# Optimization experiments

Measured on AMD Instinct MI355X. Metric: run time of the kernel, lower is better.

The kernel has to match this reference:

```python
import math
import jax, jax.numpy as jnp
import numpy as np

NUM_BINS = 8
TRANS = 8
LEFT, RIGHT = -1.0, 1.0
MIN_W = MIN_H = MIN_D = 1.0e-4


def setup_inputs() -> dict:
    key = jax.random.key(0)
    ks = jax.random.split(key, 8)
    B, D, H, OUT = 524288, 16, 256, TRANS * (3 * NUM_BINS - 1)
    x = jax.random.uniform(ks[0], (B, D), jnp.float32, -0.99, 0.99)
    W0 = jax.random.normal(ks[1], (8, H), jnp.float32) * (1.0 / math.sqrt(8))
    b0 = jnp.zeros((H,), jnp.float32)
    W1 = jax.random.normal(ks[2], (H, H), jnp.float32) * (1.0 / math.sqrt(H))
    b1 = jnp.zeros((H,), jnp.float32)
    Wout = jax.random.normal(ks[3], (H, OUT), jnp.float32) * (0.1 / math.sqrt(H))
    bout = jnp.zeros((OUT,), jnp.float32)
    return {"x": x, "W0": W0, "b0": b0, "W1": W1, "b1": b1, "Wout": Wout, "bout": bout}


def _rq_spline(x, raw_w, raw_h, raw_d):
    # x: [B, T]; raw_w/raw_h: [B, T, K]; raw_d: [B, T, K-1]
    span = RIGHT - LEFT
    const = math.log(math.exp(1.0 - MIN_D) - 1.0)
    widths = jax.nn.softmax(raw_w, axis=-1)
    heights = jax.nn.softmax(raw_h, axis=-1)
    derivs = jax.nn.softplus(raw_d + const) + MIN_D
    widths = span * (MIN_W + (1.0 - MIN_W * NUM_BINS) * widths)
    heights = span * (MIN_H + (1.0 - MIN_H * NUM_BINS) * heights)
    edge_x = LEFT + jnp.pad(jnp.cumsum(widths, axis=-1), ((0, 0), (0, 0), (1, 0)))
    edge_y = LEFT + jnp.pad(jnp.cumsum(heights, axis=-1), ((0, 0), (0, 0), (1, 0)))
    derivs = jnp.pad(derivs, ((0, 0), (0, 0), (1, 1)), constant_values=1.0)
    out_mask = (x <= LEFT + 1e-3) | (x >= RIGHT - 1e-3)
    x_in = jnp.where(out_mask, 0.0, x)
    # searchsorted(right=True) - 1 == count of edges <= x_in, minus 1
    idx = jnp.clip(jnp.sum(edge_x <= x_in[..., None], axis=-1) - 1, 0, NUM_BINS - 1)
    g = lambda a: jnp.take_along_axis(a, idx[..., None], axis=-1)[..., 0]
    xk, yk = g(edge_x), g(edge_y)
    wk, hk = g(widths), g(heights)
    dk, dk1 = g(derivs), g(derivs[..., 1:])
    sk = hk / wk
    eps = (x_in - xk) / wk
    eps_term = eps * (1.0 - eps)
    eps2 = eps * eps
    beta = sk + (dk1 + dk - 2.0 * sk) * eps_term
    alpha = hk * (sk * eps2 + dk * eps_term)
    output = jnp.where(out_mask, x, yk + alpha / beta)
    logdet = (2.0 * jnp.log(sk)
              + jnp.log(dk1 * eps2 + 2.0 * sk * eps_term + dk * (1.0 - eps) ** 2)
              - 2.0 * jnp.log(beta))
    logdet = jnp.where(out_mask, 0.0, logdet)
    return output, logdet


def reference(x, W0, b0, W1, b1, Wout, bout):
    x1 = x[..., :TRANS]   # transformed half (mask == True)
    x2 = x[..., TRANS:]   # conditioning half
    h = jax.nn.relu(x2 @ W0 + b0)
    h = jax.nn.relu(h @ W1 + b1)
    raw = (h @ Wout + bout).reshape(x.shape[0], TRANS, 3 * NUM_BINS - 1)
    raw_w = raw[..., :NUM_BINS]
    raw_h = raw[..., NUM_BINS:2 * NUM_BINS]
    raw_d = raw[..., 2 * NUM_BINS:]
    y1, logdet = _rq_spline(x1, raw_w, raw_h, raw_d)
    out = jnp.concatenate([y1, x2], axis=-1)
    return out, jnp.sum(logdet, axis=-1)
```

## Files before the change

kernel.cpp:

```cpp
#include <hip/hip_runtime.h>
#include <hip/hip_bf16.h>


typedef __bf16 bf16x8 __attribute__((ext_vector_type(8)));
typedef __bf16 bf16x4 __attribute__((ext_vector_type(4)));
typedef float  f32x4  __attribute__((ext_vector_type(4)));

#define MFMA16(a,b,c) __builtin_amdgcn_mfma_f32_16x16x32_bf16((a),(b),(c),0,0,0)

#define SW_W1_OFF 8192
#define SW_WO_OFF 73728
#define SW_TOTAL  122880

#define HSTRIDE 264

__global__ void prep_kernel(const float* __restrict__ W0,
                            const float* __restrict__ W1,
                            const float* __restrict__ Wout,
                            __bf16* __restrict__ sw)
{
  int i = blockIdx.x * 256 + threadIdx.x;
  if (i >= SW_TOTAL) return;
  const float* src; int K, N, NT, li;
  if (i < SW_W1_OFF)      { src = W0;   K = 8;   N = 256; NT = 16; li = i; }
  else if (i < SW_WO_OFF) { src = W1;   K = 256; N = 256; NT = 16; li = i - SW_W1_OFF; }
  else                    { src = Wout; K = 256; N = 184; NT = 12; li = i - SW_WO_OFF; }
  int j    = li & 7;
  int l    = (li >> 3) & 63;
  int rest = li >> 9;
  int nt   = rest % NT;
  int kb   = rest / NT;
  int k = kb * 32 + ((l >> 4) << 3) + j;
  int n = nt * 16 + (l & 15);
  float v = (k < K && n < N) ? src[k * N + n] : 0.0f;
  sw[i] = (__bf16)v;
}

__global__ __launch_bounds__(512, 4)
void fused_kernel(const float* __restrict__ x,
                  const float* __restrict__ b0v,
                  const float* __restrict__ b1v,
                  const float* __restrict__ boutv,
                  const __bf16* __restrict__ sw,
                  float* __restrict__ out,
                  int nrows)
{
  __shared__ __align__(16) unsigned char smem[2 * 64 * HSTRIDE * 2];
  __bf16* h1   = (__bf16*)smem;
  __bf16* h2   = (__bf16*)(smem + 64 * HSTRIDE * 2);
  __bf16* rawb = h1;
  float*  ldet = (float*)h2;

  const int tid  = threadIdx.x;
  const int wave = tid >> 6;
  const int lane = tid & 63;
  const int quad = lane >> 4;
  const int l16  = lane & 15;
  const int row0 = blockIdx.x * 64;

  const __bf16* swW1 = sw + SW_W1_OFF;
  const __bf16* swWo = sw + SW_WO_OFF;
  const f32x4 z4 = {0.f, 0.f, 0.f, 0.f};

  const int mq = wave >> 1;
  const int nh = wave & 1;

  {
    bf16x8 bfr[2];
    #pragma unroll
    for (int nt = 0; nt < 2; nt++){
      bf16x8 b = {};
      if (quad == 0){
        const float* xp = x + (long)(row0 + (nh*2 + nt)*16 + l16)*16 + 8;
        float4 u = *(const float4*)xp;
        float4 v = *(const float4*)(xp + 4);
        b[0]=(__bf16)u.x; b[1]=(__bf16)u.y; b[2]=(__bf16)u.z; b[3]=(__bf16)u.w;
        b[4]=(__bf16)v.x; b[5]=(__bf16)v.y; b[6]=(__bf16)v.z; b[7]=(__bf16)v.w;
      }
      bfr[nt] = b;
    }
    #pragma unroll
    for (int mi = 0; mi < 4; mi++){
      int mt = mq*4 + mi;
      bf16x8 a = *(const bf16x8*)(sw + (mt*64 + lane)*8);
      f32x4 acc0 = MFMA16(a, bfr[0], z4);
      f32x4 acc1 = MFMA16(a, bfr[1], z4);
      float4 bb = *(const float4*)(b0v + mt*16 + quad*4);
      bf16x4 p0, p1;
      p0[0]=(__bf16)fmaxf(acc0[0]+bb.x,0.f); p0[1]=(__bf16)fmaxf(acc0[1]+bb.y,0.f);
      p0[2]=(__bf16)fmaxf(acc0[2]+bb.z,0.f); p0[3]=(__bf16)fmaxf(acc0[3]+bb.w,0.f);
      p1[0]=(__bf16)fmaxf(acc1[0]+bb.x,0.f); p1[1]=(__bf16)fmaxf(acc1[1]+bb.y,0.f);
      p1[2]=(__bf16)fmaxf(acc1[2]+bb.z,0.f); p1[3]=(__bf16)fmaxf(acc1[3]+bb.w,0.f);
      *(bf16x4*)(h1 + ((nh*2+0)*16 + l16)*HSTRIDE + mt*16 + quad*4) = p0;
      *(bf16x4*)(h1 + ((nh*2+1)*16 + l16)*HSTRIDE + mt*16 + quad*4) = p1;
    }
  }
  __syncthreads();

  {
    f32x4 acc[4][2];
    #pragma unroll
    for (int mi=0;mi<4;mi++){ acc[mi][0]=z4; acc[mi][1]=z4; }
    #pragma unroll
    for (int kb=0;kb<8;kb++){
      bf16x8 bfr[2];
      #pragma unroll
      for (int nt=0;nt<2;nt++)
        bfr[nt] = *(const bf16x8*)(h1 + ((nh*2+nt)*16 + l16)*HSTRIDE + kb*32 + quad*8);
      #pragma unroll
      for (int mi=0;mi<4;mi++){
        bf16x8 a = *(const bf16x8*)(swW1 + ((kb*16 + mq*4 + mi)*64 + lane)*8);
        acc[mi][0] = MFMA16(a, bfr[0], acc[mi][0]);
        acc[mi][1] = MFMA16(a, bfr[1], acc[mi][1]);
      }
    }
    #pragma unroll
    for (int mi=0;mi<4;mi++){
      int mt = mq*4 + mi;
      float4 bb = *(const float4*)(b1v + mt*16 + quad*4);
      #pragma unroll
      for (int nt=0;nt<2;nt++){
        bf16x4 p;
        p[0]=(__bf16)fmaxf(acc[mi][nt][0]+bb.x,0.f);
        p[1]=(__bf16)fmaxf(acc[mi][nt][1]+bb.y,0.f);
        p[2]=(__bf16)fmaxf(acc[mi][nt][2]+bb.z,0.f);
        p[3]=(__bf16)fmaxf(acc[mi][nt][3]+bb.w,0.f);
        *(bf16x4*)(h2 + ((nh*2+nt)*16 + l16)*HSTRIDE + mt*16 + quad*4) = p;
      }
    }
  }
  __syncthreads();

  {
    const int mh = wave >> 2;
    const int nc = wave & 3;
    f32x4 acc[2][3];
    #pragma unroll
    for (int mi=0;mi<2;mi++)
      #pragma unroll
      for (int ni=0;ni<3;ni++) acc[mi][ni] = z4;
    #pragma unroll
    for (int kb=0;kb<8;kb++){
      bf16x8 af[2];
      #pragma unroll
      for (int mi=0;mi<2;mi++)
        af[mi] = *(const bf16x8*)(h2 + ((mh*2+mi)*16 + l16)*HSTRIDE + kb*32 + quad*8);
      #pragma unroll
      for (int ni=0;ni<3;ni++){
        bf16x8 b = *(const bf16x8*)(swWo + ((kb*12 + nc*3 + ni)*64 + lane)*8);
        acc[0][ni] = MFMA16(af[0], b, acc[0][ni]);
        acc[1][ni] = MFMA16(af[1], b, acc[1][ni]);
      }
    }
    #pragma unroll
    for (int ni=0;ni<3;ni++){
      int col = (nc*3 + ni)*16 + l16;
      if (col < 184){
        int t = (col * 713) >> 14;
        float bias = boutv[col];
        #pragma unroll
        for (int mi=0;mi<2;mi++)
          #pragma unroll
          for (int r=0;r<4;r++){
            int row = (mh*2+mi)*16 + quad*4 + r;
            rawb[row*HSTRIDE + col + t] = (__bf16)(acc[mi][ni][r] + bias);
          }
      }
    }
  }
  __syncthreads();

  {
    int row = tid >> 3;
    int t   = tid & 7;
    long gr = row0 + row;
    float xv = x[gr*16 + t];
    out[gr*16 + 8 + t] = x[gr*16 + 8 + t];

    const __bf16* rr = rawb + row*HSTRIDE + t*24;
    bf16x8 v0 = *(const bf16x8*)(rr);
    bf16x8 v1 = *(const bf16x8*)(rr + 8);
    bf16x8 v2 = *(const bf16x8*)(rr + 16);

    float ew[8], eh[8];
    float sw_ = 0.f, sh_ = 0.f;
    #pragma unroll
    for (int i=0;i<8;i++){ ew[i] = __expf((float)v0[i]); sw_ += ew[i]; }
    #pragma unroll
    for (int i=0;i<8;i++){ eh[i] = __expf((float)v1[i]); sh_ += eh[i]; }
    float cw = 1.9984f * __builtin_amdgcn_rcpf(sw_);
    float ch = 1.9984f * __builtin_amdgcn_rcpf(sh_);

    float d[9];
    d[0] = 1.f; d[8] = 1.f;
    #pragma unroll
    for (int i=0;i<7;i++){
      float z = (float)v2[i] + 0.54116666f;
      d[i+1] = fmaxf(z, 0.f) + __logf(1.f + __expf(-fabsf(z))) + 1e-4f;
    }

    bool msk = (xv <= -0.999f) || (xv >= 0.999f);
    float xin = msk ? 0.f : xv;

    float w_i = fmaf(ew[0], cw, 2e-4f);
    float h_i = fmaf(eh[0], ch, 2e-4f);
    float edge = -1.f + w_i, cy = -1.f + h_i;
    float xk = -1.f, yk = -1.f, wk = w_i, hk = h_i, dk = d[0], dk1 = d[1];
    #pragma unroll
    for (int i=1;i<8;i++){
      w_i = fmaf(ew[i], cw, 2e-4f);
      h_i = fmaf(eh[i], ch, 2e-4f);
      bool le = (edge <= xin);
      xk  = le ? edge : xk;
      yk  = le ? cy   : yk;
      wk  = le ? w_i  : wk;
      hk  = le ? h_i  : hk;
      dk  = le ? d[i] : dk;
      dk1 = le ? d[i+1] : dk1;
      edge += w_i; cy += h_i;
    }

    float rwk = __builtin_amdgcn_rcpf(wk);
    float sk  = hk * rwk;
    float eps = (xin - xk) * rwk;
    float om  = 1.f - eps;
    float et  = eps * om;
    float e2  = eps * eps;
    float beta  = sk + (dk1 + dk - 2.f*sk) * et;
    float rb    = __builtin_amdgcn_rcpf(beta);
    float alpha = hk * (sk*e2 + dk*et);
    float yv  = msk ? xv : (yk + alpha * rb);
    float num = dk1*e2 + 2.f*sk*et + dk*om*om;
    float arg = sk*sk*num*rb*rb;
    float ld  = msk ? 0.f : __logf(arg);

    out[gr*16 + t] = yv;
    ldet[tid] = ld;
  }
  __syncthreads();

  if (tid < 64){
    float s = 0.f;
    #pragma unroll
    for (int t=0;t<8;t++) s += ldet[tid*8 + t];
    out[(long)nrows*16 + row0 + tid] = s;
  }
}

extern "C" void kernel_launch(void* const* d_in, const int* in_sizes, int n_in,
                              void* d_out, int out_size, void* d_ws, size_t ws_size,
                              hipStream_t stream)
{
  const float* x    = (const float*)d_in[0];
  const float* W0   = (const float*)d_in[1];
  const float* b0   = (const float*)d_in[2];
  const float* W1   = (const float*)d_in[3];
  const float* b1   = (const float*)d_in[4];
  const float* Wout = (const float*)d_in[5];
  const float* bout = (const float*)d_in[6];
  float* out = (float*)d_out;
  __bf16* sw = (__bf16*)d_ws;

  int nrows = in_sizes[0] / 16;
  int ntiles = nrows / 64;

  prep_kernel<<<(SW_TOTAL + 255)/256, 256, 0, stream>>>(W0, W1, Wout, sw);
  fused_kernel<<<ntiles, 512, 0, stream>>>(x, b0, b1, bout, sw, out, nrows);
}
```

Baseline: 265.6 us.

## Halve rows per block to 32 and raise occupancy target to 8 blocks

Each block now processes 32 rows instead of 64. The wave-to-tile mapping is reworked so every wave covers all rows of layers 0 and 1 for two output tiles, and the output-layer tiles are split unevenly across waves (2,2,2,2,1,1,1,1). Shared memory is halved and launch bounds ask for 8 blocks per CU, aiming at more resident waves to hide latency. The spline epilogue now uses only 256 threads while the other 256 copy the passthrough half. In exchange, each weight fragment loaded from global/L2 feeds half as many MFMAs, the output layer is load-imbalanced across waves, and register pressure must fit the tighter bound.

New measurement: 276.1 us. 3.9% more time.

```diff
diff --git a/kernel.cpp b/kernel.cpp
--- a/kernel.cpp
+++ b/kernel.cpp
@@ -12,6 +12,7 @@
 #define SW_WO_OFF 73728
 #define SW_TOTAL  122880
 
+#define ROWS    32
 #define HSTRIDE 264
 
 __global__ void prep_kernel(const float* __restrict__ W0,
@@ -36,7 +37,7 @@
   sw[i] = (__bf16)v;
 }
 
-__global__ __launch_bounds__(512, 4)
+__global__ __launch_bounds__(512, 8)
 void fused_kernel(const float* __restrict__ x,
                   const float* __restrict__ b0v,
                   const float* __restrict__ b1v,
@@ -45,9 +46,9 @@
                   float* __restrict__ out,
                   int nrows)
 {
-  __shared__ __align__(16) unsigned char smem[2 * 64 * HSTRIDE * 2];
+  __shared__ __align__(16) unsigned char smem[2 * ROWS * HSTRIDE * 2];
   __bf16* h1   = (__bf16*)smem;
-  __bf16* h2   = (__bf16*)(smem + 64 * HSTRIDE * 2);
+  __bf16* h2   = (__bf16*)(smem + ROWS * HSTRIDE * 2);
   __bf16* rawb = h1;
   float*  ldet = (float*)h2;
 
@@ -56,22 +57,19 @@
   const int lane = tid & 63;
   const int quad = lane >> 4;
   const int l16  = lane & 15;
-  const int row0 = blockIdx.x * 64;
+  const int row0 = blockIdx.x * ROWS;
 
   const __bf16* swW1 = sw + SW_W1_OFF;
   const __bf16* swWo = sw + SW_WO_OFF;
   const f32x4 z4 = {0.f, 0.f, 0.f, 0.f};
 
-  const int mq = wave >> 1;
-  const int nh = wave & 1;
-
   {
     bf16x8 bfr[2];
     #pragma unroll
     for (int nt = 0; nt < 2; nt++){
       bf16x8 b = {};
       if (quad == 0){
-        const float* xp = x + (long)(row0 + (nh*2 + nt)*16 + l16)*16 + 8;
+        const float* xp = x + (long)(row0 + nt*16 + l16)*16 + 8;
         float4 u = *(const float4*)xp;
         float4 v = *(const float4*)(xp + 4);
         b[0]=(__bf16)u.x; b[1]=(__bf16)u.y; b[2]=(__bf16)u.z; b[3]=(__bf16)u.w;
@@ -80,8 +78,8 @@
       bfr[nt] = b;
     }
     #pragma unroll
-    for (int mi = 0; mi < 4; mi++){
-      int mt = mq*4 + mi;
+    for (int mi = 0; mi < 2; mi++){
+      int mt = wave*2 + mi;
       bf16x8 a = *(const bf16x8*)(sw + (mt*64 + lane)*8);
       f32x4 acc0 = MFMA16(a, bfr[0], z4);
       f32x4 acc1 = MFMA16(a, bfr[1], z4);
@@ -91,32 +89,32 @@
       p0[2]=(__bf16)fmaxf(acc0[2]+bb.z,0.f); p0[3]=(__bf16)fmaxf(acc0[3]+bb.w,0.f);
       p1[0]=(__bf16)fmaxf(acc1[0]+bb.x,0.f); p1[1]=(__bf16)fmaxf(acc1[1]+bb.y,0.f);
       p1[2]=(__bf16)fmaxf(acc1[2]+bb.z,0.f); p1[3]=(__bf16)fmaxf(acc1[3]+bb.w,0.f);
-      *(bf16x4*)(h1 + ((nh*2+0)*16 + l16)*HSTRIDE + mt*16 + quad*4) = p0;
-      *(bf16x4*)(h1 + ((nh*2+1)*16 + l16)*HSTRIDE + mt*16 + quad*4) = p1;
+      *(bf16x4*)(h1 + (0*16 + l16)*HSTRIDE + mt*16 + quad*4) = p0;
+      *(bf16x4*)(h1 + (1*16 + l16)*HSTRIDE + mt*16 + quad*4) = p1;
     }
   }
   __syncthreads();
 
   {
-    f32x4 acc[4][2];
-    #pragma unroll
-    for (int mi=0;mi<4;mi++){ acc[mi][0]=z4; acc[mi][1]=z4; }
+    f32x4 acc[2][2];
+    #pragma unroll
+    for (int mi=0;mi<2;mi++){ acc[mi][0]=z4; acc[mi][1]=z4; }
     #pragma unroll
     for (int kb=0;kb<8;kb++){
       bf16x8 bfr[2];
       #pragma unroll
       for (int nt=0;nt<2;nt++)
-        bfr[nt] = *(const bf16x8*)(h1 + ((nh*2+nt)*16 + l16)*HSTRIDE + kb*32 + quad*8);
-      #pragma unroll
-      for (int mi=0;mi<4;mi++){
-        bf16x8 a = *(const bf16x8*)(swW1 + ((kb*16 + mq*4 + mi)*64 + lane)*8);
+        bfr[nt] = *(const bf16x8*)(h1 + (nt*16 + l16)*HSTRIDE + kb*32 + quad*8);
+      #pragma unroll
+      for (int mi=0;mi<2;mi++){
+        bf16x8 a = *(const bf16x8*)(swW1 + ((kb*16 + wave*2 + mi)*64 + lane)*8);
         acc[mi][0] = MFMA16(a, bfr[0], acc[mi][0]);
         acc[mi][1] = MFMA16(a, bfr[1], acc[mi][1]);
       }
     }
     #pragma unroll
-    for (int mi=0;mi<4;mi++){
-      int mt = mq*4 + mi;
+    for (int mi=0;mi<2;mi++){
+      int mt = wave*2 + mi;
       float4 bb = *(const float4*)(b1v + mt*16 + quad*4);
       #pragma unroll
       for (int nt=0;nt<2;nt++){
@@ -125,44 +123,44 @@
         p[1]=(__bf16)fmaxf(acc[mi][nt][1]+bb.y,0.f);
         p[2]=(__bf16)fmaxf(acc[mi][nt][2]+bb.z,0.f);
         p[3]=(__bf16)fmaxf(acc[mi][nt][3]+bb.w,0.f);
-        *(bf16x4*)(h2 + ((nh*2+nt)*16 + l16)*HSTRIDE + mt*16 + quad*4) = p;
+        *(bf16x4*)(h2 + (nt*16 + l16)*HSTRIDE + mt*16 + quad*4) = p;
       }
     }
   }
   __syncthreads();
 
   {
-    const int mh = wave >> 2;
-    const int nc = wave & 3;
-    f32x4 acc[2][3];
-    #pragma unroll
-    for (int mi=0;mi<2;mi++)
-      #pragma unroll
-      for (int ni=0;ni<3;ni++) acc[mi][ni] = z4;
+    const int ncnt = (wave < 4) ? 2 : 1;
+    const int nbase = (wave < 4) ? wave*2 : wave + 4;
+    f32x4 acc[2][2];
+    #pragma unroll
+    for (int mi=0;mi<2;mi++){ acc[mi][0]=z4; acc[mi][1]=z4; }
     #pragma unroll
     for (int kb=0;kb<8;kb++){
       bf16x8 af[2];
       #pragma unroll
       for (int mi=0;mi<2;mi++)
-        af[mi] = *(const bf16x8*)(h2 + ((mh*2+mi)*16 + l16)*HSTRIDE + kb*32 + quad*8);
-      #pragma unroll
-      for (int ni=0;ni<3;ni++){
-        bf16x8 b = *(const bf16x8*)(swWo + ((kb*12 + nc*3 + ni)*64 + lane)*8);
-        acc[0][ni] = MFMA16(af[0], b, acc[0][ni]);
-        acc[1][ni] = MFMA16(af[1], b, acc[1][ni]);
-      }
-    }
-    #pragma unroll
-    for (int ni=0;ni<3;ni++){
-      int col = (nc*3 + ni)*16 + l16;
-      if (col < 184){
+        af[mi] = *(const bf16x8*)(h2 + (mi*16 + l16)*HSTRIDE + kb*32 + quad*8);
+      #pragma unroll
+      for (int ni=0;ni<2;ni++){
+        if (ni < ncnt){
+          bf16x8 b = *(const bf16x8*)(swWo + ((kb*12 + nbase + ni)*64 + lane)*8);
+          acc[0][ni] = MFMA16(af[0], b, acc[0][ni]);
+          acc[1][ni] = MFMA16(af[1], b, acc[1][ni]);
+        }
+      }
+    }
+    #pragma unroll
+    for (int ni=0;ni<2;ni++){
+      int col = (nbase + ni)*16 + l16;
+      if (ni < ncnt && col < 184){
         int t = (col * 713) >> 14;
         float bias = boutv[col];
         #pragma unroll
         for (int mi=0;mi<2;mi++)
           #pragma unroll
           for (int r=0;r<4;r++){
-            int row = (mh*2+mi)*16 + quad*4 + r;
+            int row = mi*16 + quad*4 + r;
             rawb[row*HSTRIDE + col + t] = (__bf16)(acc[mi][ni][r] + bias);
           }
       }
@@ -170,12 +168,11 @@
   }
   __syncthreads();
 
-  {
+  if (tid < 256){
     int row = tid >> 3;
     int t   = tid & 7;
     long gr = row0 + row;
     float xv = x[gr*16 + t];
-    out[gr*16 + 8 + t] = x[gr*16 + 8 + t];
 
     const __bf16* rr = rawb + row*HSTRIDE + t*24;
     bf16x8 v0 = *(const bf16x8*)(rr);
@@ -236,10 +233,15 @@
 
     out[gr*16 + t] = yv;
     ldet[tid] = ld;
-  }
-  __syncthreads();
-
-  if (tid < 64){
+  } else {
+    int p   = tid - 256;
+    long gr = row0 + (p >> 3);
+    int t   = p & 7;
+    out[gr*16 + 8 + t] = x[gr*16 + 8 + t];
+  }
+  __syncthreads();
+
+  if (tid < ROWS){
     float s = 0.f;
     #pragma unroll
     for (int t=0;t<8;t++) s += ldet[tid*8 + t];
@@ -262,7 +264,7 @@
   __bf16* sw = (__bf16*)d_ws;
 
   int nrows = in_sizes[0] / 16;
-  int ntiles = nrows / 64;
+  int ntiles = nrows / ROWS;
 
   prep_kernel<<<(SW_TOTAL + 255)/256, 256, 0, stream>>>(W0, W1, Wout, sw);
   fused_kernel<<<ntiles, 512, 0, stream>>>(x, b0, b1, bout, sw, out, nrows);
```
